# Optimization experiments

Measured on AMD Instinct MI355X. Metric: run time of the kernel, lower is better.

Reference implementation:

```python
import jax, jax.numpy as jnp
import numpy as np

B, OBS_LEN, IN_DIM, H, PRED_LEN = 32768, 8, 2, 128, 12
PRIOR_STD = 0.1
DROPOUT = 0.1


def _uni(k, shape, fan):
    b = 1.0 / np.sqrt(fan)
    return jax.random.uniform(k, shape, jnp.float32, -b, b)


def setup_inputs() -> dict:
    key = jax.random.key(0)
    ks = jax.random.split(key, 16)
    inp = {"obs_seq": jax.random.normal(ks[0], (B, OBS_LEN, IN_DIM), jnp.float32)}
    # encoder nn.LSTM params (torch init: U(-1/sqrt(H), 1/sqrt(H)))
    inp["enc_wih0"] = _uni(ks[1], (4 * H, IN_DIM), H)
    inp["enc_whh0"] = _uni(ks[2], (4 * H, H), H)
    inp["enc_bih0"] = _uni(ks[3], (4 * H,), H)
    inp["enc_bhh0"] = _uni(ks[4], (4 * H,), H)
    inp["enc_wih1"] = _uni(ks[5], (4 * H, H), H)
    inp["enc_whh1"] = _uni(ks[6], (4 * H, H), H)
    inp["enc_bih1"] = _uni(ks[7], (4 * H,), H)
    inp["enc_bhh1"] = _uni(ks[8], (4 * H,), H)
    # Bayesian decoder cell: kaiming_uniform(a=sqrt(5)) -> U(-1/sqrt(fan_in), 1/sqrt(fan_in))
    inp["din_wmu"] = _uni(ks[9], (4 * H, IN_DIM), IN_DIM)
    inp["din_wrho"] = jnp.full((4 * H, IN_DIM), -3.0, jnp.float32)
    inp["din_bmu"] = jnp.zeros((4 * H,), jnp.float32)
    inp["din_brho"] = jnp.full((4 * H,), -3.0, jnp.float32)
    inp["dhid_wmu"] = _uni(ks[10], (4 * H, H), H)
    inp["dhid_wrho"] = jnp.full((4 * H, H), -3.0, jnp.float32)
    inp["dhid_bmu"] = jnp.zeros((4 * H,), jnp.float32)
    inp["dhid_brho"] = jnp.full((4 * H,), -3.0, jnp.float32)
    # Bayesian output layer hidden -> 4
    inp["out_wmu"] = _uni(ks[11], (4, H), H)
    inp["out_wrho"] = jnp.full((4, H), -3.0, jnp.float32)
    inp["out_bmu"] = jnp.zeros((4,), jnp.float32)
    inp["out_brho"] = jnp.full((4,), -3.0, jnp.float32)
    return inp


def _lstm_layer(xs, wih, whh, bih, bhh):
    # xs: (B, T, D). PyTorch gate order: i, f, g, o.
    h0 = jnp.zeros((xs.shape[0], H), xs.dtype)
    bias = bih + bhh

    def step(carry, xt):
        h, c = carry
        g = xt @ wih.T + h @ whh.T + bias
        i, f, gg, o = jnp.split(g, 4, axis=-1)
        c = jax.nn.sigmoid(f) * c + jax.nn.sigmoid(i) * jnp.tanh(gg)
        h = jax.nn.sigmoid(o) * jnp.tanh(c)
        return (h, c), h

    (h, c), hs = jax.lax.scan(step, (h0, h0), jnp.swapaxes(xs, 0, 1))
    return jnp.swapaxes(hs, 0, 1), (h, c)


def _kl(mu, rho):
    # KL(N(mu, std^2) || N(0, PRIOR_STD^2)), std = softplus(rho)
    std = jax.nn.softplus(rho)
    return jnp.sum(jnp.log(PRIOR_STD / std) + (std * std + mu * mu) / (2.0 * PRIOR_STD * PRIOR_STD) - 0.5)


def _forward(obs_seq, enc_wih0, enc_whh0, enc_bih0, enc_bhh0,
             enc_wih1, enc_whh1, enc_bih1, enc_bhh1,
             din_wmu, din_wrho, din_bmu, din_brho,
             dhid_wmu, dhid_wrho, dhid_bmu, dhid_brho,
             out_wmu, out_wrho, out_bmu, out_brho):
    # ---- encoder (training mode: inter-layer dropout) ----
    hs0, _ = _lstm_layer(obs_seq, enc_wih0, enc_whh0, enc_bih0, enc_bhh0)
    keep = jax.random.bernoulli(jax.random.key(1), 1.0 - DROPOUT, hs0.shape)
    hs0 = jnp.where(keep, hs0 / (1.0 - DROPOUT), 0.0)
    _, (h, c) = _lstm_layer(hs0, enc_wih1, enc_whh1, enc_bih1, enc_bhh1)

    # ---- variational decoder: resample Bayesian weights every step ----
    din_wstd = jax.nn.softplus(din_wrho)
    din_bstd = jax.nn.softplus(din_brho)
    dhid_wstd = jax.nn.softplus(dhid_wrho)
    dhid_bstd = jax.nn.softplus(dhid_brho)
    out_wstd = jax.nn.softplus(out_wrho)
    out_bstd = jax.nn.softplus(out_brho)

    step_keys = jax.random.split(jax.random.key(2), PRED_LEN)

    def dstep(carry, k):
        h, c, x = carry
        k1, k2, k3, k4, k5, k6 = jax.random.split(k, 6)
        w_in = din_wmu + din_wstd * jax.random.normal(k1, din_wmu.shape, jnp.float32)
        b_in = din_bmu + din_bstd * jax.random.normal(k2, din_bmu.shape, jnp.float32)
        w_hid = dhid_wmu + dhid_wstd * jax.random.normal(k3, dhid_wmu.shape, jnp.float32)
        b_hid = dhid_bmu + dhid_bstd * jax.random.normal(k4, dhid_bmu.shape, jnp.float32)
        w_out = out_wmu + out_wstd * jax.random.normal(k5, out_wmu.shape, jnp.float32)
        b_out = out_bmu + out_bstd * jax.random.normal(k6, out_bmu.shape, jnp.float32)
        g = x @ w_in.T + h @ w_hid.T + (b_in + b_hid)
        i, f, gg, o = jnp.split(g, 4, axis=-1)
        c_new = jax.nn.sigmoid(f) * c + jax.nn.sigmoid(i) * jnp.tanh(gg)
        h_new = jax.nn.sigmoid(o) * jnp.tanh(c_new)
        out = h_new @ w_out.T + b_out
        mu_xy = out[:, :2]
        log_sigma = jnp.clip(out[:, 2:], -4.0, 2.0)
        return (h_new, c_new, mu_xy), (mu_xy, log_sigma)

    _, (mus, lss) = jax.lax.scan(dstep, (h, c, obs_seq[:, -1, :]), step_keys)
    mu = jnp.swapaxes(mus, 0, 1)        # (B, pred_len, 2)
    log_sigma = jnp.swapaxes(lss, 0, 1)  # (B, pred_len, 2)

    # KL is overwritten each step; since std/mu are eps-independent it equals the analytic sum
    kl = (_kl(din_wmu, din_wrho) + _kl(din_bmu, din_brho)
          + _kl(dhid_wmu, dhid_wrho) + _kl(dhid_bmu, dhid_brho)
          + _kl(out_wmu, out_wrho) + _kl(out_bmu, out_brho))
    return mu, log_sigma, kl


def reference(obs_seq, enc_wih0, enc_whh0, enc_bih0, enc_bhh0,
              enc_wih1, enc_whh1, enc_bih1, enc_bhh1,
              din_wmu, din_wrho, din_bmu, din_brho,
              dhid_wmu, dhid_wrho, dhid_bmu, dhid_brho,
              out_wmu, out_wrho, out_bmu, out_brho):
    return _forward(obs_seq, enc_wih0, enc_whh0, enc_bih0, enc_bhh0,
                    enc_wih1, enc_whh1, enc_bih1, enc_bhh1,
                    din_wmu, din_wrho, din_bmu, din_brho,
                    dhid_wmu, dhid_wrho, dhid_bmu, dhid_brho,
                    out_wmu, out_wrho, out_bmu, out_brho)
```

## Files before the change

### kernel.cpp

```cpp
#include <hip/hip_runtime.h>

typedef float f32x4 __attribute__((ext_vector_type(4)));
typedef short bf16x8 __attribute__((ext_vector_type(8)));
typedef unsigned short ushort_t;

__device__ __forceinline__ unsigned rotl32(unsigned x, unsigned r){ return (x << r) | (x >> (32u - r)); }

__device__ __forceinline__ void tf2x32(unsigned k0, unsigned k1, unsigned c0, unsigned c1,
                                       unsigned &o0, unsigned &o1){
  unsigned ks2 = k0 ^ k1 ^ 0x1BD11BDAu;
  unsigned x0 = c0 + k0, x1 = c1 + k1;
#define TFR(r) { x0 += x1; x1 = rotl32(x1, r); x1 ^= x0; }
  TFR(13) TFR(15) TFR(26) TFR(6)
  x0 += k1;  x1 += ks2 + 1u;
  TFR(17) TFR(29) TFR(16) TFR(24)
  x0 += ks2; x1 += k0 + 2u;
  TFR(13) TFR(15) TFR(26) TFR(6)
  x0 += k0;  x1 += k1 + 3u;
  TFR(17) TFR(29) TFR(16) TFR(24)
  x0 += k1;  x1 += ks2 + 4u;
  TFR(13) TFR(15) TFR(26) TFR(6)
  x0 += ks2; x1 += k0 + 5u;
#undef TFR
  o0 = x0; o1 = x1;
}

__device__ __forceinline__ float bits_to_u01(unsigned bits){
  return __uint_as_float((bits >> 9) | 0x3f800000u) - 1.0f;
}

__device__ __forceinline__ float erfinv_f(float x){
  float w = -log1pf(-x * x);
  float p;
  if (w < 5.0f){
    w -= 2.5f;
    p = 2.81022636e-08f;
    p = 3.43273939e-07f + p * w;
    p = -3.5233877e-06f + p * w;
    p = -4.39150654e-06f + p * w;
    p = 0.00021858087f + p * w;
    p = -0.00125372503f + p * w;
    p = -0.00417768164f + p * w;
    p = 0.246640727f + p * w;
    p = 1.50140941f + p * w;
  } else {
    w = sqrtf(w) - 3.0f;
    p = -0.000200214257f;
    p = 0.000100950558f + p * w;
    p = 0.00134934322f + p * w;
    p = -0.00367342844f + p * w;
    p = 0.00573950773f + p * w;
    p = -0.0076224613f + p * w;
    p = 0.00943887047f + p * w;
    p = 1.00167406f + p * w;
    p = 2.83297682f + p * w;
  }
  return p * x;
}

__device__ __forceinline__ ushort_t f2bf(float f){
  unsigned u = __float_as_uint(f);
  unsigned r = u + 0x7fffu + ((u >> 16) & 1u);
  return (ushort_t)(r >> 16);
}
__device__ __forceinline__ float bf2f(ushort_t h){ return __uint_as_float(((unsigned)h) << 16); }

__device__ __forceinline__ float sigmf(float x){
  return __builtin_amdgcn_rcpf(1.0f + __expf(-x));
}
__device__ __forceinline__ float tanhf_(float x){
  float e = __expf(-2.0f * fabsf(x));
  float t = (1.0f - e) * __builtin_amdgcn_rcpf(1.0f + e);
  return copysignf(t, x);
}

constexpr int BT = 64;
constexpr int PITCH = 136;

__global__ void prep_enc(const float* __restrict__ whh0, const float* __restrict__ wih1,
                         const float* __restrict__ whh1,
                         const float* __restrict__ bih0, const float* __restrict__ bhh0,
                         const float* __restrict__ bih1, const float* __restrict__ bhh1,
                         ushort_t* __restrict__ o0, ushort_t* __restrict__ o1, ushort_t* __restrict__ o2,
                         float* __restrict__ bias0, float* __restrict__ bias1){
  int tid = blockIdx.x * 256 + threadIdx.x;
  if (tid < 65536)        o0[tid] = f2bf(whh0[tid]);
  else if (tid < 131072)  o1[tid - 65536] = f2bf(wih1[tid - 65536]);
  else if (tid < 196608)  o2[tid - 131072] = f2bf(whh1[tid - 131072]);
  else if (tid < 197120){ int j = tid - 196608; bias0[j] = bih0[j] + bhh0[j]; }
  else if (tid < 197632){ int j = tid - 197120; bias1[j] = bih1[j] + bhh1[j]; }
}

__global__ void prep_dec(
    const float* __restrict__ din_wmu, const float* __restrict__ din_wrho,
    const float* __restrict__ din_bmu, const float* __restrict__ din_brho,
    const float* __restrict__ dhid_wmu, const float* __restrict__ dhid_wrho,
    const float* __restrict__ dhid_bmu, const float* __restrict__ dhid_brho,
    const float* __restrict__ out_wmu, const float* __restrict__ out_wrho,
    const float* __restrict__ out_bmu, const float* __restrict__ out_brho,
    ushort_t* __restrict__ dwhid, float* __restrict__ dwin, float* __restrict__ dbin,
    float* __restrict__ dbhid, float* __restrict__ dwout, float* __restrict__ dbout){
  int tid = blockIdx.x * 256 + threadIdx.x;
  if (tid >= 12 * 68100) return;
  int s = tid / 68100, r = tid - s * 68100;
  unsigned sk0, sk1, gk0, gk1, b0, b1;
  tf2x32(0u, 2u, 0u, (unsigned)s, sk0, sk1);
  int g, e; const float *mu, *rho;
  if (r < 1024)      { g = 0; e = r;          mu = din_wmu;  rho = din_wrho;  }
  else if (r < 1536) { g = 1; e = r - 1024;   mu = din_bmu;  rho = din_brho;  }
  else if (r < 67072){ g = 2; e = r - 1536;   mu = dhid_wmu; rho = dhid_wrho; }
  else if (r < 67584){ g = 3; e = r - 67072;  mu = dhid_bmu; rho = dhid_brho; }
  else if (r < 68096){ g = 4; e = r - 67584;  mu = out_wmu;  rho = out_wrho;  }
  else               { g = 5; e = r - 68096;  mu = out_bmu;  rho = out_brho;  }
  tf2x32(sk0, sk1, 0u, (unsigned)g, gk0, gk1);
  tf2x32(gk0, gk1, 0u, (unsigned)e, b0, b1);
  unsigned bits = b0 ^ b1;
  float u01 = bits_to_u01(bits);
  const float LO = __uint_as_float(0xBF7FFFFFu);
  float u = u01 * 2.0f + LO;
  u = fmaxf(LO, u);
  float eps = 1.41421356237f * erfinv_f(u);
  float stdv = log1pf(expf(rho[e]));
  float val = mu[e] + stdv * eps;
  switch (g){
    case 0:  dwin [s * 1024 + e] = val; break;
    case 1:  dbin [s * 512  + e] = val; break;
    case 2:  dwhid[s * 65536 + e] = f2bf(val); break;
    case 3:  dbhid[s * 512  + e] = val; break;
    case 4:  dwout[s * 512  + e] = val; break;
    default: dbout[s * 4    + e] = val; break;
  }
}

__global__ void gen_mask(unsigned* __restrict__ maskw){
  unsigned w = blockIdx.x * 256 + threadIdx.x;
  unsigned word = 0;
  #pragma unroll 4
  for (int b = 0; b < 32; ++b){
    unsigned o0, o1;
    tf2x32(0u, 1u, 0u, w * 32u + (unsigned)b, o0, o1);
    unsigned bits = o0 ^ o1;
    float u = bits_to_u01(bits);
    word |= (u < 0.9f ? 1u : 0u) << b;
  }
  maskw[w] = word;
}

__global__ void kl_kernel(
    const float* __restrict__ m0, const float* __restrict__ r0,
    const float* __restrict__ m1, const float* __restrict__ r1,
    const float* __restrict__ m2, const float* __restrict__ r2,
    const float* __restrict__ m3, const float* __restrict__ r3,
    const float* __restrict__ m4, const float* __restrict__ r4,
    const float* __restrict__ m5, const float* __restrict__ r5,
    float* __restrict__ out){
  __shared__ float red[1024];
  int tid = threadIdx.x;
  float s = 0.f;
  auto term = [](float mu, float rho){
    float stdv = log1pf(expf(rho));
    return logf(0.1f / stdv) + (stdv * stdv + mu * mu) * 50.0f - 0.5f;
  };
  for (int i = tid; i < 1024;  i += 1024) s += term(m0[i], r0[i]);
  for (int i = tid; i < 512;   i += 1024) s += term(m1[i], r1[i]);
  for (int i = tid; i < 65536; i += 1024) s += term(m2[i], r2[i]);
  for (int i = tid; i < 512;   i += 1024) s += term(m3[i], r3[i]);
  for (int i = tid; i < 512;   i += 1024) s += term(m4[i], r4[i]);
  if (tid < 4) s += term(m5[tid], r5[tid]);
  red[tid] = s;
  __syncthreads();
  for (int off = 512; off > 0; off >>= 1){
    if (tid < off) red[tid] += red[tid + off];
    __syncthreads();
  }
  if (tid == 0) out[1572864] = red[0];
}

__device__ __forceinline__ void gemm_k128(const ushort_t* __restrict__ Hlds,
                                          const ushort_t* __restrict__ W,
                                          int wv, int lx, int lg, f32x4 acc[4][4]){
  #pragma unroll
  for (int ki = 0; ki < 4; ++ki){
    bf16x8 a[4];
    #pragma unroll
    for (int mt = 0; mt < 4; ++mt)
      a[mt] = *(const bf16x8*)(Hlds + (16 * mt + lx) * PITCH + 32 * ki + 8 * lg);
    #pragma unroll
    for (int g = 0; g < 4; ++g){
      bf16x8 b = *(const bf16x8*)(W + (128 * g + 16 * wv + lx) * 128 + 32 * ki + 8 * lg);
      #pragma unroll
      for (int mt = 0; mt < 4; ++mt)
        acc[g][mt] = __builtin_amdgcn_mfma_f32_16x16x32_bf16(a[mt], b, acc[g][mt], 0, 0, 0);
    }
  }
}

__global__ __launch_bounds__(512, 2) void lstm_main(
    const float* __restrict__ obs,
    const float* __restrict__ wih0,
    const ushort_t* __restrict__ whh0,
    const ushort_t* __restrict__ wih1,
    const ushort_t* __restrict__ whh1,
    const float* __restrict__ bias0,
    const float* __restrict__ bias1,
    const ushort_t* __restrict__ dwhid,
    const float* __restrict__ dwin,
    const float* __restrict__ dbin,
    const float* __restrict__ dbhid,
    const float* __restrict__ dwout,
    const float* __restrict__ dbout,
    const unsigned* __restrict__ maskw,
    float* __restrict__ out){
  __shared__ __align__(16) ushort_t H0s[BT * PITCH];
  __shared__ __align__(16) ushort_t HDs[BT * PITCH];
  __shared__ __align__(16) ushort_t H1s[BT * PITCH];
  __shared__ float OBSs[BT * 16];
  __shared__ float XDs[BT * 2];

  const int tid = threadIdx.x;
  const int wv = tid >> 6;
  const int l  = tid & 63;
  const int lx = l & 15;
  const int lg = l >> 4;
  const int b0 = blockIdx.x * BT;
  const int hj = 16 * wv + lx;

  for (int i = tid; i < BT * 16; i += 512) OBSs[i] = obs[b0 * 16 + i];
  for (int i = tid; i < BT * PITCH; i += 512){ H0s[i] = 0; H1s[i] = 0; }

  float c0v[16], c1v[16];
  #pragma unroll
  for (int i = 0; i < 16; ++i){ c0v[i] = 0.f; c1v[i] = 0.f; }

  float b0g[4], b1g[4], wx0g[4], wx1g[4];
  #pragma unroll
  for (int g = 0; g < 4; ++g){
    int j = 128 * g + hj;
    b0g[g] = bias0[j]; b1g[g] = bias1[j];
    wx0g[g] = wih0[2 * j]; wx1g[g] = wih0[2 * j + 1];
  }
  __syncthreads();

  f32x4 acc[4][4];
  const f32x4 zero4 = {0.f, 0.f, 0.f, 0.f};

  for (int t = 0; t < 8; ++t){
    #pragma unroll
    for (int g = 0; g < 4; ++g)
      #pragma unroll
      for (int mt = 0; mt < 4; ++mt) acc[g][mt] = zero4;
    gemm_k128(H0s, whh0, wv, lx, lg, acc);
    __syncthreads();
    #pragma unroll
    for (int mt = 0; mt < 4; ++mt){
      #pragma unroll
      for (int e = 0; e < 4; ++e){
        int r = 16 * mt + 4 * lg + e;
        float x0 = OBSs[r * 16 + 2 * t], x1 = OBSs[r * 16 + 2 * t + 1];
        float gi = acc[0][mt][e] + b0g[0] + x0 * wx0g[0] + x1 * wx1g[0];
        float gf = acc[1][mt][e] + b0g[1] + x0 * wx0g[1] + x1 * wx1g[1];
        float gg = acc[2][mt][e] + b0g[2] + x0 * wx0g[2] + x1 * wx1g[2];
        float go = acc[3][mt][e] + b0g[3] + x0 * wx0g[3] + x1 * wx1g[3];
        float cn = sigmf(gf) * c0v[4 * mt + e] + sigmf(gi) * tanhf_(gg);
        c0v[4 * mt + e] = cn;
        float hn = sigmf(go) * tanhf_(cn);
        H0s[r * PITCH + hj] = f2bf(hn);
        unsigned idx = ((unsigned)(b0 + r) << 10) | ((unsigned)t << 7) | (unsigned)hj;
        unsigned keep = (maskw[idx >> 5] >> (idx & 31u)) & 1u;
        HDs[r * PITCH + hj] = f2bf(keep ? hn * (1.0f / 0.9f) : 0.0f);
      }
    }
    __syncthreads();
    #pragma unroll
    for (int g = 0; g < 4; ++g)
      #pragma unroll
      for (int mt = 0; mt < 4; ++mt) acc[g][mt] = zero4;
    gemm_k128(HDs, wih1, wv, lx, lg, acc);
    gemm_k128(H1s, whh1, wv, lx, lg, acc);
    __syncthreads();
    #pragma unroll
    for (int mt = 0; mt < 4; ++mt){
      #pragma unroll
      for (int e = 0; e < 4; ++e){
        int r = 16 * mt + 4 * lg + e;
        float gi = acc[0][mt][e] + b1g[0];
        float gf = acc[1][mt][e] + b1g[1];
        float gg = acc[2][mt][e] + b1g[2];
        float go = acc[3][mt][e] + b1g[3];
        float cn = sigmf(gf) * c1v[4 * mt + e] + sigmf(gi) * tanhf_(gg);
        c1v[4 * mt + e] = cn;
        float hn = sigmf(go) * tanhf_(cn);
        H1s[r * PITCH + hj] = f2bf(hn);
      }
    }
    __syncthreads();
  }

  if (tid < 128) XDs[tid] = OBSs[(tid >> 1) * 16 + 14 + (tid & 1)];
  __syncthreads();

  for (int s = 0; s < 12; ++s){
    #pragma unroll
    for (int g = 0; g < 4; ++g)
      #pragma unroll
      for (int mt = 0; mt < 4; ++mt) acc[g][mt] = zero4;
    gemm_k128(H1s, dwhid + s * 65536, wv, lx, lg, acc);
    __syncthreads();
    const float* bin  = dbin  + s * 512;
    const float* bhid = dbhid + s * 512;
    const float* win  = dwin  + s * 1024;
    float bg[4], wa[4], wb[4];
    #pragma unroll
    for (int g = 0; g < 4; ++g){
      int j = 128 * g + hj;
      bg[g] = bin[j] + bhid[j];
      wa[g] = win[2 * j]; wb[g] = win[2 * j + 1];
    }
    #pragma unroll
    for (int mt = 0; mt < 4; ++mt){
      #pragma unroll
      for (int e = 0; e < 4; ++e){
        int r = 16 * mt + 4 * lg + e;
        float x0 = XDs[2 * r], x1 = XDs[2 * r + 1];
        float gi = acc[0][mt][e] + bg[0] + x0 * wa[0] + x1 * wb[0];
        float gf = acc[1][mt][e] + bg[1] + x0 * wa[1] + x1 * wb[1];
        float gg = acc[2][mt][e] + bg[2] + x0 * wa[2] + x1 * wb[2];
        float go = acc[3][mt][e] + bg[3] + x0 * wa[3] + x1 * wb[3];
        float cn = sigmf(gf) * c1v[4 * mt + e] + sigmf(gi) * tanhf_(gg);
        c1v[4 * mt + e] = cn;
        float hn = sigmf(go) * tanhf_(cn);
        H1s[r * PITCH + hj] = f2bf(hn);
      }
    }
    __syncthreads();
    if (tid < 256){
      int r = tid >> 2, o = tid & 3;
      const float* wo = dwout + s * 512 + o * 128;
      float sum = dbout[s * 4 + o];
      #pragma unroll 8
      for (int k = 0; k < 128; ++k) sum += bf2f(H1s[r * PITCH + k]) * wo[k];
      int gb = b0 + r;
      if (o < 2){
        out[gb * 24 + s * 2 + o] = sum;
        XDs[2 * r + o] = sum;
      } else {
        float ls = fminf(fmaxf(sum, -4.0f), 2.0f);
        out[786432 + gb * 24 + s * 2 + (o - 2)] = ls;
      }
    }
    __syncthreads();
  }
}

extern "C" void kernel_launch(void* const* d_in, const int* in_sizes, int n_in,
                              void* d_out, int out_size, void* d_ws, size_t ws_size,
                              hipStream_t stream){
  (void)in_sizes; (void)n_in; (void)out_size; (void)ws_size;
  const float* obs   = (const float*)d_in[0];
  const float* wih0  = (const float*)d_in[1];
  const float* whh0f = (const float*)d_in[2];
  const float* bih0  = (const float*)d_in[3];
  const float* bhh0  = (const float*)d_in[4];
  const float* wih1f = (const float*)d_in[5];
  const float* whh1f = (const float*)d_in[6];
  const float* bih1  = (const float*)d_in[7];
  const float* bhh1  = (const float*)d_in[8];
  const float* din_wmu  = (const float*)d_in[9];
  const float* din_wrho = (const float*)d_in[10];
  const float* din_bmu  = (const float*)d_in[11];
  const float* din_brho = (const float*)d_in[12];
  const float* dhid_wmu  = (const float*)d_in[13];
  const float* dhid_wrho = (const float*)d_in[14];
  const float* dhid_bmu  = (const float*)d_in[15];
  const float* dhid_brho = (const float*)d_in[16];
  const float* out_wmu  = (const float*)d_in[17];
  const float* out_wrho = (const float*)d_in[18];
  const float* out_bmu  = (const float*)d_in[19];
  const float* out_brho = (const float*)d_in[20];

  char* wsb = (char*)d_ws;
  ushort_t* whh0b = (ushort_t*)(wsb + 0);
  ushort_t* wih1b = (ushort_t*)(wsb + 131072);
  ushort_t* whh1b = (ushort_t*)(wsb + 262144);
  float* bias0    = (float*)(wsb + 393216);
  float* bias1    = (float*)(wsb + 395264);
  ushort_t* dwhid = (ushort_t*)(wsb + 397312);
  float* dwin     = (float*)(wsb + 1970176);
  float* dbin     = (float*)(wsb + 2019328);
  float* dbhid    = (float*)(wsb + 2043904);
  float* dwout    = (float*)(wsb + 2068480);
  float* dbout    = (float*)(wsb + 2093056);
  unsigned* maskw = (unsigned*)(wsb + 2093248);

  prep_enc<<<772, 256, 0, stream>>>(whh0f, wih1f, whh1f, bih0, bhh0, bih1, bhh1,
                                    whh0b, wih1b, whh1b, bias0, bias1);
  prep_dec<<<(12 * 68100 + 255) / 256, 256, 0, stream>>>(
      din_wmu, din_wrho, din_bmu, din_brho,
      dhid_wmu, dhid_wrho, dhid_bmu, dhid_brho,
      out_wmu, out_wrho, out_bmu, out_brho,
      dwhid, dwin, dbin, dbhid, dwout, dbout);
  gen_mask<<<4096, 256, 0, stream>>>(maskw);
  kl_kernel<<<1, 1024, 0, stream>>>(din_wmu, din_wrho, din_bmu, din_brho,
                                    dhid_wmu, dhid_wrho, dhid_bmu, dhid_brho,
                                    out_wmu, out_wrho, out_bmu, out_brho,
                                    (float*)d_out);
  lstm_main<<<512, 512, 0, stream>>>(obs, wih0, whh0b, wih1b, whh1b, bias0, bias1,
                                     dwhid, dwin, dbin, dbhid, dwout, dbout, maskw,
                                     (float*)d_out);
}
```

Measured before the change: 882.9 us.

## Fuse prep kernels, fold inputs and biases into GEMM K, reshape LSTM tiling

Merges the four preprocessing kernels into one launch. The input projection and summed biases are folded into extra K columns of the bf16 weight matrices, so obs and dropout-scaled inputs ride through the MFMA GEMM instead of scalar FMAs. The main kernel drops to 256 threads with each wave owning 32 hidden units and software-pipelines the B-operand loads. The dropout mask is laid out transposed for vector loads, the cell state is packed as bf16 pairs, and a fused sigmoid*tanh formula is used. The change adds rounding of inputs, biases and cell state to bf16, which may cost accuracy.

```diff
diff --git a/kernel.cpp b/kernel.cpp
--- a/kernel.cpp
+++ b/kernel.cpp
@@ -3,6 +3,7 @@
 typedef float f32x4 __attribute__((ext_vector_type(4)));
 typedef short bf16x8 __attribute__((ext_vector_type(8)));
 typedef unsigned short ushort_t;
+typedef unsigned int uint_t;
 
 __device__ __forceinline__ unsigned rotl32(unsigned x, unsigned r){ return (x << r) | (x >> (32u - r)); }
 
@@ -65,157 +66,199 @@
 }
 __device__ __forceinline__ float bf2f(ushort_t h){ return __uint_as_float(((unsigned)h) << 16); }
 
-__device__ __forceinline__ float sigmf(float x){
-  return __builtin_amdgcn_rcpf(1.0f + __expf(-x));
-}
-__device__ __forceinline__ float tanhf_(float x){
-  float e = __expf(-2.0f * fabsf(x));
-  float t = (1.0f - e) * __builtin_amdgcn_rcpf(1.0f + e);
-  return copysignf(t, x);
+__device__ __forceinline__ float norm_draw(unsigned sk0, unsigned sk1, unsigned g, unsigned e){
+  unsigned gk0, gk1, b0, b1;
+  tf2x32(sk0, sk1, 0u, g, gk0, gk1);
+  tf2x32(gk0, gk1, 0u, e, b0, b1);
+  unsigned bits = b0 ^ b1;
+  float u01 = bits_to_u01(bits);
+  const float LO = __uint_as_float(0xBF7FFFFFu);
+  float u = u01 * 2.0f + LO;
+  u = fmaxf(LO, u);
+  return 1.41421356237f * erfinv_f(u);
 }
 
 constexpr int BT = 64;
-constexpr int PITCH = 136;
-
-__global__ void prep_enc(const float* __restrict__ whh0, const float* __restrict__ wih1,
-                         const float* __restrict__ whh1,
-                         const float* __restrict__ bih0, const float* __restrict__ bhh0,
-                         const float* __restrict__ bih1, const float* __restrict__ bhh1,
-                         ushort_t* __restrict__ o0, ushort_t* __restrict__ o1, ushort_t* __restrict__ o2,
-                         float* __restrict__ bias0, float* __restrict__ bias1){
-  int tid = blockIdx.x * 256 + threadIdx.x;
-  if (tid < 65536)        o0[tid] = f2bf(whh0[tid]);
-  else if (tid < 131072)  o1[tid - 65536] = f2bf(wih1[tid - 65536]);
-  else if (tid < 196608)  o2[tid - 131072] = f2bf(whh1[tid - 131072]);
-  else if (tid < 197120){ int j = tid - 196608; bias0[j] = bih0[j] + bhh0[j]; }
-  else if (tid < 197632){ int j = tid - 197120; bias1[j] = bih1[j] + bhh1[j]; }
-}
-
-__global__ void prep_dec(
+constexpr int PITCH = 168;
+constexpr int WROW_E = 160;
+
+
+__global__ void prep_all(
+    const float* __restrict__ wih0,  const float* __restrict__ whh0,
+    const float* __restrict__ bih0,  const float* __restrict__ bhh0,
+    const float* __restrict__ wih1,  const float* __restrict__ whh1,
+    const float* __restrict__ bih1,  const float* __restrict__ bhh1,
     const float* __restrict__ din_wmu, const float* __restrict__ din_wrho,
     const float* __restrict__ din_bmu, const float* __restrict__ din_brho,
     const float* __restrict__ dhid_wmu, const float* __restrict__ dhid_wrho,
     const float* __restrict__ dhid_bmu, const float* __restrict__ dhid_brho,
     const float* __restrict__ out_wmu, const float* __restrict__ out_wrho,
     const float* __restrict__ out_bmu, const float* __restrict__ out_brho,
-    ushort_t* __restrict__ dwhid, float* __restrict__ dwin, float* __restrict__ dbin,
-    float* __restrict__ dbhid, float* __restrict__ dwout, float* __restrict__ dbout){
-  int tid = blockIdx.x * 256 + threadIdx.x;
-  if (tid >= 12 * 68100) return;
-  int s = tid / 68100, r = tid - s * 68100;
-  unsigned sk0, sk1, gk0, gk1, b0, b1;
-  tf2x32(0u, 2u, 0u, (unsigned)s, sk0, sk1);
-  int g, e; const float *mu, *rho;
-  if (r < 1024)      { g = 0; e = r;          mu = din_wmu;  rho = din_wrho;  }
-  else if (r < 1536) { g = 1; e = r - 1024;   mu = din_bmu;  rho = din_brho;  }
-  else if (r < 67072){ g = 2; e = r - 1536;   mu = dhid_wmu; rho = dhid_wrho; }
-  else if (r < 67584){ g = 3; e = r - 67072;  mu = dhid_bmu; rho = dhid_brho; }
-  else if (r < 68096){ g = 4; e = r - 67584;  mu = out_wmu;  rho = out_wrho;  }
-  else               { g = 5; e = r - 68096;  mu = out_bmu;  rho = out_brho;  }
-  tf2x32(sk0, sk1, 0u, (unsigned)g, gk0, gk1);
-  tf2x32(gk0, gk1, 0u, (unsigned)e, b0, b1);
-  unsigned bits = b0 ^ b1;
-  float u01 = bits_to_u01(bits);
-  const float LO = __uint_as_float(0xBF7FFFFFu);
-  float u = u01 * 2.0f + LO;
-  u = fmaxf(LO, u);
-  float eps = 1.41421356237f * erfinv_f(u);
-  float stdv = log1pf(expf(rho[e]));
-  float val = mu[e] + stdv * eps;
-  switch (g){
-    case 0:  dwin [s * 1024 + e] = val; break;
-    case 1:  dbin [s * 512  + e] = val; break;
-    case 2:  dwhid[s * 65536 + e] = f2bf(val); break;
-    case 3:  dbhid[s * 512  + e] = val; break;
-    case 4:  dwout[s * 512  + e] = val; break;
-    default: dbout[s * 4    + e] = val; break;
-  }
-}
-
-__global__ void gen_mask(unsigned* __restrict__ maskw){
-  unsigned w = blockIdx.x * 256 + threadIdx.x;
-  unsigned word = 0;
-  #pragma unroll 4
-  for (int b = 0; b < 32; ++b){
-    unsigned o0, o1;
-    tf2x32(0u, 1u, 0u, w * 32u + (unsigned)b, o0, o1);
-    unsigned bits = o0 ^ o1;
-    float u = bits_to_u01(bits);
-    word |= (u < 0.9f ? 1u : 0u) << b;
-  }
-  maskw[w] = word;
-}
-
-__global__ void kl_kernel(
-    const float* __restrict__ m0, const float* __restrict__ r0,
-    const float* __restrict__ m1, const float* __restrict__ r1,
-    const float* __restrict__ m2, const float* __restrict__ r2,
-    const float* __restrict__ m3, const float* __restrict__ r3,
-    const float* __restrict__ m4, const float* __restrict__ r4,
-    const float* __restrict__ m5, const float* __restrict__ r5,
-    float* __restrict__ out){
-  __shared__ float red[1024];
-  int tid = threadIdx.x;
-  float s = 0.f;
-  auto term = [](float mu, float rho){
-    float stdv = log1pf(expf(rho));
-    return logf(0.1f / stdv) + (stdv * stdv + mu * mu) * 50.0f - 0.5f;
-  };
-  for (int i = tid; i < 1024;  i += 1024) s += term(m0[i], r0[i]);
-  for (int i = tid; i < 512;   i += 1024) s += term(m1[i], r1[i]);
-  for (int i = tid; i < 65536; i += 1024) s += term(m2[i], r2[i]);
-  for (int i = tid; i < 512;   i += 1024) s += term(m3[i], r3[i]);
-  for (int i = tid; i < 512;   i += 1024) s += term(m4[i], r4[i]);
-  if (tid < 4) s += term(m5[tid], r5[tid]);
-  red[tid] = s;
-  __syncthreads();
-  for (int off = 512; off > 0; off >>= 1){
-    if (tid < off) red[tid] += red[tid + off];
-    __syncthreads();
-  }
-  if (tid == 0) out[1572864] = red[0];
-}
-
-__device__ __forceinline__ void gemm_k128(const ushort_t* __restrict__ Hlds,
-                                          const ushort_t* __restrict__ W,
-                                          int wv, int lx, int lg, f32x4 acc[4][4]){
+    ushort_t* __restrict__ whh0e, ushort_t* __restrict__ wih1e, ushort_t* __restrict__ whh1b,
+    ushort_t* __restrict__ dwhide, float* __restrict__ dwout, float* __restrict__ dbout,
+    unsigned* __restrict__ maskT, float* __restrict__ out){
+  const int blk = blockIdx.x, tid = threadIdx.x;
+
+  if (blk < 4096){
+    unsigned w = blk * 256u + tid;
+    unsigned t = w >> 17, h = (w >> 10) & 127u, bw = w & 1023u;
+    unsigned word = 0;
+    #pragma unroll 4
+    for (int i = 0; i < 32; ++i){
+      unsigned ctr = (bw * 32u + i) * 1024u + t * 128u + h;
+      unsigned o0, o1;
+      tf2x32(0u, 1u, 0u, ctr, o0, o1);
+      float u = bits_to_u01(o0 ^ o1);
+      word |= (u < 0.9f ? 1u : 0u) << i;
+    }
+    maskT[w] = word;
+  } else if (blk < 4992){
+    int idx = (blk - 4096) * 256 + tid;
+    if (idx < 81920){
+      int row = idx / 160, col = idx - row * 160;
+      float v;
+      if (col < 128)       v = whh0[row * 128 + col];
+      else if (col == 128) v = wih0[row * 2];
+      else if (col == 129) v = wih0[row * 2 + 1];
+      else if (col == 130) v = bih0[row] + bhh0[row];
+      else                 v = 0.0f;
+      whh0e[idx] = f2bf(v);
+    } else if (idx < 163840){
+      int j = idx - 81920;
+      int row = j / 160, col = j - row * 160;
+      float v;
+      if (col < 128)       v = wih1[row * 128 + col];
+      else if (col == 130) v = bih1[row] + bhh1[row];
+      else                 v = 0.0f;
+      wih1e[j] = f2bf(v);
+    } else {
+      int j = idx - 163840;
+      whh1b[j] = f2bf(whh1[j]);
+    }
+  } else if (blk < 8857){
+    int idx = (blk - 4992) * 256 + tid;
+    if (idx >= 12 * 82436) return;
+    int s = idx / 82436, r = idx - s * 82436;
+    unsigned sk0, sk1;
+    tf2x32(0u, 2u, 0u, (unsigned)s, sk0, sk1);
+    if (r < 81920){
+      int row = r / 160, col = r - row * 160;
+      float v;
+      if (col < 128){
+        unsigned e = (unsigned)(row * 128 + col);
+        v = dhid_wmu[e] + log1pf(expf(dhid_wrho[e])) * norm_draw(sk0, sk1, 2u, e);
+      } else if (col == 128){
+        unsigned e = (unsigned)(row * 2);
+        v = din_wmu[e] + log1pf(expf(din_wrho[e])) * norm_draw(sk0, sk1, 0u, e);
+      } else if (col == 129){
+        unsigned e = (unsigned)(row * 2 + 1);
+        v = din_wmu[e] + log1pf(expf(din_wrho[e])) * norm_draw(sk0, sk1, 0u, e);
+      } else if (col == 130){
+        unsigned e = (unsigned)row;
+        float v1 = din_bmu[e]  + log1pf(expf(din_brho[e]))  * norm_draw(sk0, sk1, 1u, e);
+        float v2 = dhid_bmu[e] + log1pf(expf(dhid_brho[e])) * norm_draw(sk0, sk1, 3u, e);
+        v = v1 + v2;
+      } else v = 0.0f;
+      dwhide[s * 81920 + r] = f2bf(v);
+    } else if (r < 82432){
+      unsigned e = (unsigned)(r - 81920);
+      dwout[s * 512 + e] = out_wmu[e] + log1pf(expf(out_wrho[e])) * norm_draw(sk0, sk1, 4u, e);
+    } else {
+      unsigned e = (unsigned)(r - 82432);
+      dbout[s * 4 + e] = out_bmu[e] + log1pf(expf(out_brho[e])) * norm_draw(sk0, sk1, 5u, e);
+    }
+  } else {
+    __shared__ float red[256];
+    float s = 0.f;
+    auto term = [](float mu, float rho){
+      float stdv = log1pf(expf(rho));
+      return logf(0.1f / stdv) + (stdv * stdv + mu * mu) * 50.0f - 0.5f;
+    };
+    for (int i = tid; i < 1024;  i += 256) s += term(din_wmu[i], din_wrho[i]);
+    for (int i = tid; i < 512;   i += 256) s += term(din_bmu[i], din_brho[i]);
+    for (int i = tid; i < 65536; i += 256) s += term(dhid_wmu[i], dhid_wrho[i]);
+    for (int i = tid; i < 512;   i += 256) s += term(dhid_bmu[i], dhid_brho[i]);
+    for (int i = tid; i < 512;   i += 256) s += term(out_wmu[i], out_wrho[i]);
+    if (tid < 4) s += term(out_bmu[tid], out_brho[tid]);
+    red[tid] = s;
+    __syncthreads();
+    for (int off = 128; off > 0; off >>= 1){
+      if (tid < off) red[tid] += red[tid + off];
+      __syncthreads();
+    }
+    if (tid == 0) out[1572864] = red[0];
+  }
+}
+
+__device__ __forceinline__ float lstm_elem(float gi, float gf, float gg, float go, float& c){
+  float sf = __builtin_amdgcn_rcpf(1.0f + __expf(-gf));
+  float Ei = __expf(-gi);
+  float Eg = __expf(2.0f * gg);
+  float itanh = (Eg - 1.0f) * __builtin_amdgcn_rcpf((1.0f + Ei) * (Eg + 1.0f));
+  float cn = sf * c + itanh;
+  c = cn;
+  float Eo = __expf(-go);
+  float Ec = __expf(2.0f * cn);
+  return (Ec - 1.0f) * __builtin_amdgcn_rcpf((1.0f + Eo) * (Ec + 1.0f));
+}
+
+template<int NKI, int WROW>
+__device__ __forceinline__ void gemm_T(const ushort_t* __restrict__ H,
+                                       const ushort_t* __restrict__ W,
+                                       int wv, int lx, int lg, f32x4 (&acc)[4][2][4]){
+  const ushort_t* wp = W + (32 * wv + lx) * WROW + 8 * lg;
+  const ushort_t* hp = H + lx * PITCH + 8 * lg;
+  bf16x8 B[3][4];
   #pragma unroll
-  for (int ki = 0; ki < 4; ++ki){
-    bf16x8 a[4];
+  for (int c = 0; c < 3; ++c){
+    int ki = c >> 1, wc = c & 1;
     #pragma unroll
-    for (int mt = 0; mt < 4; ++mt)
-      a[mt] = *(const bf16x8*)(Hlds + (16 * mt + lx) * PITCH + 32 * ki + 8 * lg);
+    for (int g = 0; g < 4; ++g)
+      B[c][g] = *(const bf16x8*)(wp + (128 * g + 16 * wc) * WROW + 32 * ki);
+  }
+  bf16x8 a[4];
+  #pragma unroll
+  for (int c = 0; c < 2 * NKI; ++c){
+    int ki = c >> 1, wc = c & 1;
+    if (wc == 0){
+      #pragma unroll
+      for (int m = 0; m < 4; ++m)
+        a[m] = *(const bf16x8*)(hp + 16 * m * PITCH + 32 * ki);
+    }
     #pragma unroll
-    for (int g = 0; g < 4; ++g){
-      bf16x8 b = *(const bf16x8*)(W + (128 * g + 16 * wv + lx) * 128 + 32 * ki + 8 * lg);
-      #pragma unroll
-      for (int mt = 0; mt < 4; ++mt)
-        acc[g][mt] = __builtin_amdgcn_mfma_f32_16x16x32_bf16(a[mt], b, acc[g][mt], 0, 0, 0);
-    }
-  }
-}
-
-__global__ __launch_bounds__(512, 2) void lstm_main(
+    for (int g = 0; g < 4; ++g)
+      #pragma unroll
+      for (int m = 0; m < 4; ++m)
+        acc[g][wc][m] = __builtin_amdgcn_mfma_f32_16x16x32_bf16(a[m], B[c % 3][g], acc[g][wc][m], 0, 0, 0);
+    if (c + 3 < 2 * NKI){
+      int ki2 = (c + 3) >> 1, wc2 = (c + 3) & 1;
+      #pragma unroll
+      for (int g = 0; g < 4; ++g)
+        B[c % 3][g] = *(const bf16x8*)(wp + (128 * g + 16 * wc2) * WROW + 32 * ki2);
+    }
+  }
+}
+
+__device__ __forceinline__ float cp_lo(unsigned w){ return __uint_as_float(w << 16); }
+__device__ __forceinline__ float cp_hi(unsigned w){ return __uint_as_float(w & 0xFFFF0000u); }
+__device__ __forceinline__ unsigned cp_pack(float lo, float hi){
+  return (__float_as_uint(hi) & 0xFFFF0000u) | (__float_as_uint(lo) >> 16);
+}
+
+__global__ __launch_bounds__(256, 2) void lstm_main(
     const float* __restrict__ obs,
-    const float* __restrict__ wih0,
-    const ushort_t* __restrict__ whh0,
-    const ushort_t* __restrict__ wih1,
-    const ushort_t* __restrict__ whh1,
-    const float* __restrict__ bias0,
-    const float* __restrict__ bias1,
-    const ushort_t* __restrict__ dwhid,
-    const float* __restrict__ dwin,
-    const float* __restrict__ dbin,
-    const float* __restrict__ dbhid,
+    const ushort_t* __restrict__ whh0e,
+    const ushort_t* __restrict__ wih1e,
+    const ushort_t* __restrict__ whh1b,
+    const ushort_t* __restrict__ dwhide,
     const float* __restrict__ dwout,
     const float* __restrict__ dbout,
-    const unsigned* __restrict__ maskw,
+    const unsigned* __restrict__ maskT,
     float* __restrict__ out){
-  __shared__ __align__(16) ushort_t H0s[BT * PITCH];
-  __shared__ __align__(16) ushort_t HDs[BT * PITCH];
-  __shared__ __align__(16) ushort_t H1s[BT * PITCH];
-  __shared__ float OBSs[BT * 16];
-  __shared__ float XDs[BT * 2];
+  __shared__ __align__(16) ushort_t sm[3 * BT * PITCH];
+  ushort_t* H0 = sm;
+  ushort_t* HD = sm + BT * PITCH;
+  ushort_t* H1 = sm + 2 * BT * PITCH;
 
   const int tid = threadIdx.x;
   const int wv = tid >> 6;
@@ -223,129 +266,144 @@
   const int lx = l & 15;
   const int lg = l >> 4;
   const int b0 = blockIdx.x * BT;
-  const int hj = 16 * wv + lx;
-
-  for (int i = tid; i < BT * 16; i += 512) OBSs[i] = obs[b0 * 16 + i];
-  for (int i = tid; i < BT * PITCH; i += 512){ H0s[i] = 0; H1s[i] = 0; }
-
-  float c0v[16], c1v[16];
+
+  {
+    uint_t* p = (uint_t*)sm;
+    for (int i = tid; i < 3 * BT * PITCH / 2; i += 256) p[i] = 0;
+  }
+  __syncthreads();
+  if (tid < 192){
+    int buf = tid / 64, r = tid & 63;
+    sm[buf * BT * PITCH + r * PITCH + 130] = (ushort_t)0x3F80;
+  }
+  if (tid < 128){
+    int r = tid >> 1, c = tid & 1;
+    H0[r * PITCH + 128 + c] = f2bf(obs[(b0 + r) * 16 + c]);
+  }
+  unsigned c0p[16], c1p[16];
   #pragma unroll
-  for (int i = 0; i < 16; ++i){ c0v[i] = 0.f; c1v[i] = 0.f; }
-
-  float b0g[4], b1g[4], wx0g[4], wx1g[4];
-  #pragma unroll
-  for (int g = 0; g < 4; ++g){
-    int j = 128 * g + hj;
-    b0g[g] = bias0[j]; b1g[g] = bias1[j];
-    wx0g[g] = wih0[2 * j]; wx1g[g] = wih0[2 * j + 1];
-  }
+  for (int i = 0; i < 16; ++i){ c0p[i] = 0; c1p[i] = 0; }
   __syncthreads();
 
-  f32x4 acc[4][4];
+  f32x4 acc[4][2][4];
   const f32x4 zero4 = {0.f, 0.f, 0.f, 0.f};
+#define ZERO_ACC() { _Pragma("unroll") for (int g=0;g<4;++g) _Pragma("unroll") for (int wc=0;wc<2;++wc) _Pragma("unroll") for (int m=0;m<4;++m) acc[g][wc][m]=zero4; }
 
   for (int t = 0; t < 8; ++t){
+    ZERO_ACC();
+    gemm_T<5, WROW_E>(H0, whh0e, wv, lx, lg, acc);
+    __syncthreads();
+    {
+      uint2 mk[2];
+      #pragma unroll
+      for (int wc = 0; wc < 2; ++wc){
+        int hj = 32 * wv + 16 * wc + lx;
+        mk[wc] = *(const uint2*)(maskT + (unsigned)t * 131072u + (unsigned)hj * 1024u + (unsigned)(blockIdx.x * 2));
+      }
+      #pragma unroll
+      for (int wc = 0; wc < 2; ++wc){
+        int hj = 32 * wv + 16 * wc + lx;
+        #pragma unroll
+        for (int m = 0; m < 4; ++m){
+          unsigned mbits = (m & 2) ? mk[wc].y : mk[wc].x;
+          #pragma unroll
+          for (int ep = 0; ep < 2; ++ep){
+            unsigned cw = c0p[wc * 8 + m * 2 + ep];
+            float cv0 = cp_lo(cw), cv1 = cp_hi(cw);
+            int e0 = 2 * ep, r0 = 16 * m + 4 * lg + e0;
+            float h0v = lstm_elem(acc[0][wc][m][e0], acc[1][wc][m][e0], acc[2][wc][m][e0], acc[3][wc][m][e0], cv0);
+            float h1v = lstm_elem(acc[0][wc][m][e0+1], acc[1][wc][m][e0+1], acc[2][wc][m][e0+1], acc[3][wc][m][e0+1], cv1);
+            c0p[wc * 8 + m * 2 + ep] = cp_pack(cv0, cv1);
+            H0[r0 * PITCH + hj] = f2bf(h0v);
+            H0[(r0 + 1) * PITCH + hj] = f2bf(h1v);
+            unsigned k0 = (mbits >> (r0 & 31)) & 1u;
+            unsigned k1 = (mbits >> ((r0 + 1) & 31)) & 1u;
+            HD[r0 * PITCH + hj] = k0 ? f2bf(h0v * (1.0f / 0.9f)) : (ushort_t)0;
+            HD[(r0 + 1) * PITCH + hj] = k1 ? f2bf(h1v * (1.0f / 0.9f)) : (ushort_t)0;
+          }
+        }
+      }
+    }
+    __syncthreads();
+    ZERO_ACC();
+    gemm_T<5, WROW_E>(HD, wih1e, wv, lx, lg, acc);
+    gemm_T<4, 128>(H1, whh1b, wv, lx, lg, acc);
+    __syncthreads();
     #pragma unroll
-    for (int g = 0; g < 4; ++g)
-      #pragma unroll
-      for (int mt = 0; mt < 4; ++mt) acc[g][mt] = zero4;
-    gemm_k128(H0s, whh0, wv, lx, lg, acc);
+    for (int wc = 0; wc < 2; ++wc){
+      int hj = 32 * wv + 16 * wc + lx;
+      #pragma unroll
+      for (int m = 0; m < 4; ++m){
+        #pragma unroll
+        for (int ep = 0; ep < 2; ++ep){
+          unsigned cw = c1p[wc * 8 + m * 2 + ep];
+          float cv0 = cp_lo(cw), cv1 = cp_hi(cw);
+          int e0 = 2 * ep, r0 = 16 * m + 4 * lg + e0;
+          float h0v = lstm_elem(acc[0][wc][m][e0], acc[1][wc][m][e0], acc[2][wc][m][e0], acc[3][wc][m][e0], cv0);
+          float h1v = lstm_elem(acc[0][wc][m][e0+1], acc[1][wc][m][e0+1], acc[2][wc][m][e0+1], acc[3][wc][m][e0+1], cv1);
+          c1p[wc * 8 + m * 2 + ep] = cp_pack(cv0, cv1);
+          H1[r0 * PITCH + hj] = f2bf(h0v);
+          H1[(r0 + 1) * PITCH + hj] = f2bf(h1v);
+        }
+      }
+    }
+    if (t < 7 && tid < 128){
+      int r = tid >> 1, c = tid & 1;
+      H0[r * PITCH + 128 + c] = f2bf(obs[(b0 + r) * 16 + 2 * (t + 1) + c]);
+    }
+    __syncthreads();
+  }
+
+  if (tid < 128){
+    int r = tid >> 1, c = tid & 1;
+    H1[r * PITCH + 128 + c] = f2bf(obs[(b0 + r) * 16 + 14 + c]);
+  }
+  __syncthreads();
+
+  for (int s = 0; s < 12; ++s){
+    ZERO_ACC();
+    gemm_T<5, WROW_E>(H1, dwhide + s * 81920, wv, lx, lg, acc);
     __syncthreads();
     #pragma unroll
-    for (int mt = 0; mt < 4; ++mt){
-      #pragma unroll
-      for (int e = 0; e < 4; ++e){
-        int r = 16 * mt + 4 * lg + e;
-        float x0 = OBSs[r * 16 + 2 * t], x1 = OBSs[r * 16 + 2 * t + 1];
-        float gi = acc[0][mt][e] + b0g[0] + x0 * wx0g[0] + x1 * wx1g[0];
-        float gf = acc[1][mt][e] + b0g[1] + x0 * wx0g[1] + x1 * wx1g[1];
-        float gg = acc[2][mt][e] + b0g[2] + x0 * wx0g[2] + x1 * wx1g[2];
-        float go = acc[3][mt][e] + b0g[3] + x0 * wx0g[3] + x1 * wx1g[3];
-        float cn = sigmf(gf) * c0v[4 * mt + e] + sigmf(gi) * tanhf_(gg);
-        c0v[4 * mt + e] = cn;
-        float hn = sigmf(go) * tanhf_(cn);
-        H0s[r * PITCH + hj] = f2bf(hn);
-        unsigned idx = ((unsigned)(b0 + r) << 10) | ((unsigned)t << 7) | (unsigned)hj;
-        unsigned keep = (maskw[idx >> 5] >> (idx & 31u)) & 1u;
-        HDs[r * PITCH + hj] = f2bf(keep ? hn * (1.0f / 0.9f) : 0.0f);
-      }
-    }
-    __syncthreads();
-    #pragma unroll
-    for (int g = 0; g < 4; ++g)
-      #pragma unroll
-      for (int mt = 0; mt < 4; ++mt) acc[g][mt] = zero4;
-    gemm_k128(HDs, wih1, wv, lx, lg, acc);
-    gemm_k128(H1s, whh1, wv, lx, lg, acc);
-    __syncthreads();
-    #pragma unroll
-    for (int mt = 0; mt < 4; ++mt){
-      #pragma unroll
-      for (int e = 0; e < 4; ++e){
-        int r = 16 * mt + 4 * lg + e;
-        float gi = acc[0][mt][e] + b1g[0];
-        float gf = acc[1][mt][e] + b1g[1];
-        float gg = acc[2][mt][e] + b1g[2];
-        float go = acc[3][mt][e] + b1g[3];
-        float cn = sigmf(gf) * c1v[4 * mt + e] + sigmf(gi) * tanhf_(gg);
-        c1v[4 * mt + e] = cn;
-        float hn = sigmf(go) * tanhf_(cn);
-        H1s[r * PITCH + hj] = f2bf(hn);
-      }
-    }
-    __syncthreads();
-  }
-
-  if (tid < 128) XDs[tid] = OBSs[(tid >> 1) * 16 + 14 + (tid & 1)];
-  __syncthreads();
-
-  for (int s = 0; s < 12; ++s){
-    #pragma unroll
-    for (int g = 0; g < 4; ++g)
-      #pragma unroll
-      for (int mt = 0; mt < 4; ++mt) acc[g][mt] = zero4;
-    gemm_k128(H1s, dwhid + s * 65536, wv, lx, lg, acc);
-    __syncthreads();
-    const float* bin  = dbin  + s * 512;
-    const float* bhid = dbhid + s * 512;
-    const float* win  = dwin  + s * 1024;
-    float bg[4], wa[4], wb[4];
-    #pragma unroll
-    for (int g = 0; g < 4; ++g){
-      int j = 128 * g + hj;
-      bg[g] = bin[j] + bhid[j];
-      wa[g] = win[2 * j]; wb[g] = win[2 * j + 1];
-    }
-    #pragma unroll
-    for (int mt = 0; mt < 4; ++mt){
-      #pragma unroll
-      for (int e = 0; e < 4; ++e){
-        int r = 16 * mt + 4 * lg + e;
-        float x0 = XDs[2 * r], x1 = XDs[2 * r + 1];
-        float gi = acc[0][mt][e] + bg[0] + x0 * wa[0] + x1 * wb[0];
-        float gf = acc[1][mt][e] + bg[1] + x0 * wa[1] + x1 * wb[1];
-        float gg = acc[2][mt][e] + bg[2] + x0 * wa[2] + x1 * wb[2];
-        float go = acc[3][mt][e] + bg[3] + x0 * wa[3] + x1 * wb[3];
-        float cn = sigmf(gf) * c1v[4 * mt + e] + sigmf(gi) * tanhf_(gg);
-        c1v[4 * mt + e] = cn;
-        float hn = sigmf(go) * tanhf_(cn);
-        H1s[r * PITCH + hj] = f2bf(hn);
-      }
-    }
-    __syncthreads();
-    if (tid < 256){
+    for (int wc = 0; wc < 2; ++wc){
+      int hj = 32 * wv + 16 * wc + lx;
+      #pragma unroll
+      for (int m = 0; m < 4; ++m){
+        #pragma unroll
+        for (int ep = 0; ep < 2; ++ep){
+          unsigned cw = c1p[wc * 8 + m * 2 + ep];
+          float cv0 = cp_lo(cw), cv1 = cp_hi(cw);
+          int e0 = 2 * ep, r0 = 16 * m + 4 * lg + e0;
+          float h0v = lstm_elem(acc[0][wc][m][e0], acc[1][wc][m][e0], acc[2][wc][m][e0], acc[3][wc][m][e0], cv0);
+          float h1v = lstm_elem(acc[0][wc][m][e0+1], acc[1][wc][m][e0+1], acc[2][wc][m][e0+1], acc[3][wc][m][e0+1], cv1);
+          c1p[wc * 8 + m * 2 + ep] = cp_pack(cv0, cv1);
+          H1[r0 * PITCH + hj] = f2bf(h0v);
+          H1[(r0 + 1) * PITCH + hj] = f2bf(h1v);
+        }
+      }
+    }
+    __syncthreads();
+    {
       int r = tid >> 2, o = tid & 3;
       const float* wo = dwout + s * 512 + o * 128;
       float sum = dbout[s * 4 + o];
-      #pragma unroll 8
-      for (int k = 0; k < 128; ++k) sum += bf2f(H1s[r * PITCH + k]) * wo[k];
+      const ushort_t* hrow = H1 + r * PITCH;
+      #pragma unroll
+      for (int k = 0; k < 128; k += 8){
+        bf16x8 hv = *(const bf16x8*)(hrow + k);
+        f32x4 wa = *(const f32x4*)(wo + k);
+        f32x4 wb = *(const f32x4*)(wo + k + 4);
+        sum += bf2f((ushort_t)hv[0]) * wa[0] + bf2f((ushort_t)hv[1]) * wa[1]
+             + bf2f((ushort_t)hv[2]) * wa[2] + bf2f((ushort_t)hv[3]) * wa[3]
+             + bf2f((ushort_t)hv[4]) * wb[0] + bf2f((ushort_t)hv[5]) * wb[1]
+             + bf2f((ushort_t)hv[6]) * wb[2] + bf2f((ushort_t)hv[7]) * wb[3];
+      }
       int gb = b0 + r;
       if (o < 2){
         out[gb * 24 + s * 2 + o] = sum;
-        XDs[2 * r + o] = sum;
+        H1[r * PITCH + 128 + o] = f2bf(sum);
       } else {
-        float ls = fminf(fmaxf(sum, -4.0f), 2.0f);
-        out[786432 + gb * 24 + s * 2 + (o - 2)] = ls;
+        out[786432 + gb * 24 + s * 2 + (o - 2)] = fminf(fmaxf(sum, -4.0f), 2.0f);
       }
     }
     __syncthreads();
@@ -358,11 +416,11 @@
   (void)in_sizes; (void)n_in; (void)out_size; (void)ws_size;
   const float* obs   = (const float*)d_in[0];
   const float* wih0  = (const float*)d_in[1];
-  const float* whh0f = (const float*)d_in[2];
+  const float* whh0  = (const float*)d_in[2];
   const float* bih0  = (const float*)d_in[3];
   const float* bhh0  = (const float*)d_in[4];
-  const float* wih1f = (const float*)d_in[5];
-  const float* whh1f = (const float*)d_in[6];
+  const float* wih1  = (const float*)d_in[5];
+  const float* whh1  = (const float*)d_in[6];
   const float* bih1  = (const float*)d_in[7];
   const float* bhh1  = (const float*)d_in[8];
   const float* din_wmu  = (const float*)d_in[9];
@@ -379,32 +437,21 @@
   const float* out_brho = (const float*)d_in[20];
 
   char* wsb = (char*)d_ws;
-  ushort_t* whh0b = (ushort_t*)(wsb + 0);
-  ushort_t* wih1b = (ushort_t*)(wsb + 131072);
-  ushort_t* whh1b = (ushort_t*)(wsb + 262144);
-  float* bias0    = (float*)(wsb + 393216);
-  float* bias1    = (float*)(wsb + 395264);
-  ushort_t* dwhid = (ushort_t*)(wsb + 397312);
-  float* dwin     = (float*)(wsb + 1970176);
-  float* dbin     = (float*)(wsb + 2019328);
-  float* dbhid    = (float*)(wsb + 2043904);
-  float* dwout    = (float*)(wsb + 2068480);
-  float* dbout    = (float*)(wsb + 2093056);
-  unsigned* maskw = (unsigned*)(wsb + 2093248);
-
-  prep_enc<<<772, 256, 0, stream>>>(whh0f, wih1f, whh1f, bih0, bhh0, bih1, bhh1,
-                                    whh0b, wih1b, whh1b, bias0, bias1);
-  prep_dec<<<(12 * 68100 + 255) / 256, 256, 0, stream>>>(
+  ushort_t* whh0e  = (ushort_t*)(wsb + 0);
+  ushort_t* wih1e  = (ushort_t*)(wsb + 163840);
+  ushort_t* whh1b  = (ushort_t*)(wsb + 327680);
+  ushort_t* dwhide = (ushort_t*)(wsb + 458752);
+  float*    dwout  = (float*)(wsb + 2424832);
+  float*    dbout  = (float*)(wsb + 2449408);
+  unsigned* maskT  = (unsigned*)(wsb + 2449600);
+
+  prep_all<<<8858, 256, 0, stream>>>(
+      wih0, whh0, bih0, bhh0, wih1, whh1, bih1, bhh1,
       din_wmu, din_wrho, din_bmu, din_brho,
       dhid_wmu, dhid_wrho, dhid_bmu, dhid_brho,
       out_wmu, out_wrho, out_bmu, out_brho,
-      dwhid, dwin, dbin, dbhid, dwout, dbout);
-  gen_mask<<<4096, 256, 0, stream>>>(maskw);
-  kl_kernel<<<1, 1024, 0, stream>>>(din_wmu, din_wrho, din_bmu, din_brho,
-                                    dhid_wmu, dhid_wrho, dhid_bmu, dhid_brho,
-                                    out_wmu, out_wrho, out_bmu, out_brho,
-                                    (float*)d_out);
-  lstm_main<<<512, 512, 0, stream>>>(obs, wih0, whh0b, wih1b, whh1b, bias0, bias1,
-                                     dwhid, dwin, dbin, dbhid, dwout, dbout, maskw,
-                                     (float*)d_out);
-}
+      whh0e, wih1e, whh1b, dwhide, dwout, dbout, maskT, (float*)d_out);
+
+  lstm_main<<<512, 256, 0, stream>>>(obs, whh0e, wih1e, whh1b, dwhide, dwout, dbout,
+                                     maskT, (float*)d_out);
+}
```

New measurement: 1.120 ms. 1.27x slower.
